# Kernel optimization log

Hardware: AMD Instinct MI355X
Metric: run time of the kernel (lower is better)

The kernel has to match this reference:

```python
import jax, jax.numpy as jnp
import numpy as np

WINDOW_SIZE = 64
SHIFT_SIZE = WINDOW_SIZE // 2  # shift_windows=True
HEAD_DIM = 64
SCALE = HEAD_DIM ** (-0.5)


def _shift_mask(W):
    # static shift-window mask, computed with numpy (all shapes static)
    img_mask = np.zeros((W,), dtype=np.float32)
    cnt = 0
    for s in (slice(0, -WINDOW_SIZE), slice(-WINDOW_SIZE, -SHIFT_SIZE), slice(-SHIFT_SIZE, None)):
        img_mask[s] = cnt
        cnt += 1
    mw = img_mask.reshape(W // WINDOW_SIZE, WINDOW_SIZE)  # (num_win, ws)
    mask = mw[:, None, :] - mw[:, :, None]                # (num_win, ws, ws)
    mask = np.where(mask != 0.0, -100.0, 0.0).astype(np.float32)
    return jnp.asarray(mask)


def setup_inputs() -> dict:
    key = jax.random.key(0)
    k1, k2, k3, k4 = jax.random.split(key, 4)
    B, W, C = 32, 8192, HEAD_DIM
    return {
        "q": jax.random.normal(k1, (B, W, C), dtype=jnp.float32),
        "k": jax.random.normal(k2, (B, W, C), dtype=jnp.float32),
        "v": jax.random.normal(k3, (B, W, C), dtype=jnp.float32),
        "rel_pos_table": jax.random.normal(k4, (2 * WINDOW_SIZE - 1, 1), dtype=jnp.float32) * 0.02,
    }


def reference(q, k, v, rel_pos_table):
    B, W, C = q.shape
    ws = WINDOW_SIZE
    # relative position bias gather: (1, ws, ws)
    coords = jnp.arange(ws)
    rel_idx = coords[None, :] * 0 + (coords[:, None] - coords[None, :]) + (ws - 1)  # (ws, ws)
    bias = rel_pos_table[rel_idx.reshape(-1)].reshape(ws, ws, -1)
    bias = jnp.transpose(bias, (2, 0, 1))  # (1, ws, ws)

    mask = _shift_mask(W)  # (num_win, ws, ws)

    # cyclic shift
    q = jnp.roll(q, shift=-SHIFT_SIZE, axis=1)
    k = jnp.roll(k, shift=-SHIFT_SIZE, axis=1)
    v = jnp.roll(v, shift=-SHIFT_SIZE, axis=1)

    # window partition -> (B * num_win, ws, C)
    num_win = W // ws
    qw = q.reshape(B * num_win, ws, C)
    kw = k.reshape(B * num_win, ws, C)
    vw = v.reshape(B * num_win, ws, C)

    attn = jnp.einsum('bnc,bmc->bnm', qw, kw) * SCALE + bias  # (B*nw, ws, ws)
    attn = attn.reshape(B, num_win, ws, ws) + mask[None]
    attn = attn.reshape(-1, ws, ws)
    attn = jax.nn.softmax(attn, axis=-1)

    xw = jnp.einsum('bnm,bmc->bnc', attn, vw)  # (B*nw, ws, C)
    x = xw.reshape(B, W, C)
    x = jnp.roll(x, shift=SHIFT_SIZE, axis=1)
    return (x, attn)
```

## Files before the change

kernel.cpp:

```cpp
#include <hip/hip_runtime.h>
#include <cstdint>
#include <cstddef>

#define WS 64
#define SHIFT 32
#define WTOT 8192
#define NWIN 128
#define NWPB 8
#define NBLK 512
#define SCALE_F 0.125f

typedef __bf16 bf16x8 __attribute__((ext_vector_type(8)));
typedef __bf16 bf16x4 __attribute__((ext_vector_type(4)));
typedef float f32x4 __attribute__((ext_vector_type(4)));

__device__ __forceinline__ int swz16(int row, int col) {
  return (row * WS + col) ^ (((row >> 1) & 7) << 3);
}

__global__ __launch_bounds__(256, 2) void win_attn(
    const float* __restrict__ q, const float* __restrict__ k,
    const float* __restrict__ v, const float* __restrict__ table,
    float* __restrict__ xout, float* __restrict__ attn_out) {
  __shared__ __align__(16) unsigned short s_mem[2][4 * WS * WS];

  const int t = threadIdx.x;
  const int bid = blockIdx.x;
  const int lane = t & 63;
  const int wave = t >> 6;
  const int lrow = lane & 15;
  const int quad = lane >> 4;

  const int klr = t >> 2;
  const int klc = (t & 3) << 4;
  const int vm0 = (t >> 4) << 2;
  const int vc0 = (t & 15) << 2;

  float biasr[4][4];
  {
    const float* tb = table + (WS - 1);
#pragma unroll
    for (int reg = 0; reg < 4; ++reg) {
      const int r = wave * 16 + quad * 4 + reg;
#pragma unroll
      for (int j = 0; j < 4; ++j) {
        biasr[reg][j] = __ldg(tb + (r - (j * 16 + lrow)));
      }
    }
  }

  float4 L[2][12];

#define ISSUE(W)                                                          \
  {                                                                       \
    const int wid_ = bid * NWPB + (W);                                    \
    const int ba_ = wid_ >> 7;                                            \
    const int wi_ = wid_ & (NWIN - 1);                                    \
    const size_t base_ = (size_t)ba_ * WTOT;                              \
    const int qr_ = (wi_ * WS + wave * 16 + lrow + SHIFT) & (WTOT - 1);   \
    const float* qp_ = q + (base_ + qr_) * WS + quad * 8;                 \
    L[(W) & 1][0] = *(const float4*)(qp_);                                \
    L[(W) & 1][1] = *(const float4*)(qp_ + 4);                            \
    L[(W) & 1][2] = *(const float4*)(qp_ + 32);                           \
    L[(W) & 1][3] = *(const float4*)(qp_ + 36);                           \
    const int kr_ = (wi_ * WS + klr + SHIFT) & (WTOT - 1);                \
    const float* kp_ = k + (base_ + kr_) * WS + klc;                      \
    L[(W) & 1][4] = *(const float4*)(kp_);                                \
    L[(W) & 1][5] = *(const float4*)(kp_ + 4);                            \
    L[(W) & 1][6] = *(const float4*)(kp_ + 8);                            \
    L[(W) & 1][7] = *(const float4*)(kp_ + 12);                           \
    const int vr0_ = (wi_ * WS + vm0 + 0 + SHIFT) & (WTOT - 1);           \
    const int vr1_ = (wi_ * WS + vm0 + 1 + SHIFT) & (WTOT - 1);           \
    const int vr2_ = (wi_ * WS + vm0 + 2 + SHIFT) & (WTOT - 1);           \
    const int vr3_ = (wi_ * WS + vm0 + 3 + SHIFT) & (WTOT - 1);           \
    L[(W) & 1][8]  = *(const float4*)(v + (base_ + vr0_) * WS + vc0);     \
    L[(W) & 1][9]  = *(const float4*)(v + (base_ + vr1_) * WS + vc0);     \
    L[(W) & 1][10] = *(const float4*)(v + (base_ + vr2_) * WS + vc0);     \
    L[(W) & 1][11] = *(const float4*)(v + (base_ + vr3_) * WS + vc0);     \
  }

  ISSUE(0);

#pragma unroll
  for (int w = 0; w < NWPB; ++w) {
    const int s = w & 1;
    unsigned short* const s_khi  = s_mem[s];
    unsigned short* const s_klo  = s_mem[s] + WS * WS;
    unsigned short* const s_vthi = s_mem[s] + 2 * WS * WS;
    unsigned short* const s_vtlo = s_mem[s] + 3 * WS * WS;

    const int wid = bid * NWPB + w;
    const int batch = wid >> 7;
    const int win = wid & (NWIN - 1);
    const bool masked = (win == NWIN - 1);
    const size_t base = (size_t)batch * WTOT;

    if (w + 1 < NWPB) ISSUE(w + 1);

    {
      const float a[16] = {L[s][4].x, L[s][4].y, L[s][4].z, L[s][4].w,
                           L[s][5].x, L[s][5].y, L[s][5].z, L[s][5].w,
                           L[s][6].x, L[s][6].y, L[s][6].z, L[s][6].w,
                           L[s][7].x, L[s][7].y, L[s][7].z, L[s][7].w};
#pragma unroll
      for (int h = 0; h < 2; ++h) {
        bf16x8 hv, lv;
#pragma unroll
        for (int e = 0; e < 8; ++e) {
          const float x = a[8 * h + e];
          const __bf16 hh = (__bf16)x;
          hv[e] = hh;
          lv[e] = (__bf16)(x - (float)hh);
        }
        const int idx = swz16(klr, klc + 8 * h);
        *(bf16x8*)(s_khi + idx) = hv;
        *(bf16x8*)(s_klo + idx) = lv;
      }
    }
    {
      const float vb[4][4] = {
          {L[s][8].x,  L[s][8].y,  L[s][8].z,  L[s][8].w},
          {L[s][9].x,  L[s][9].y,  L[s][9].z,  L[s][9].w},
          {L[s][10].x, L[s][10].y, L[s][10].z, L[s][10].w},
          {L[s][11].x, L[s][11].y, L[s][11].z, L[s][11].w}};
#pragma unroll
      for (int e = 0; e < 4; ++e) {
        bf16x4 hv, lv;
#pragma unroll
        for (int j = 0; j < 4; ++j) {
          const float x = vb[j][e];
          const __bf16 hh = (__bf16)x;
          hv[j] = hh;
          lv[j] = (__bf16)(x - (float)hh);
        }
        const int idx = swz16(vc0 + e, vm0);
        *(bf16x4*)(s_vthi + idx) = hv;
        *(bf16x4*)(s_vtlo + idx) = lv;
      }
    }
    bf16x8 qfhi[2], qflo[2];
#pragma unroll
    for (int kh = 0; kh < 2; ++kh) {
      const float a[8] = {L[s][2 * kh].x,     L[s][2 * kh].y,
                          L[s][2 * kh].z,     L[s][2 * kh].w,
                          L[s][2 * kh + 1].x, L[s][2 * kh + 1].y,
                          L[s][2 * kh + 1].z, L[s][2 * kh + 1].w};
      bf16x8 hv, lv;
#pragma unroll
      for (int e = 0; e < 8; ++e) {
        const __bf16 hh = (__bf16)a[e];
        hv[e] = hh;
        lv[e] = (__bf16)(a[e] - (float)hh);
      }
      qfhi[kh] = hv;
      qflo[kh] = lv;
    }

    __syncthreads();

    const f32x4 z4 = {0.f, 0.f, 0.f, 0.f};
    f32x4 acc[4] = {z4, z4, z4, z4};
#pragma unroll
    for (int kh = 0; kh < 2; ++kh) {
      const int k0 = kh * 32 + quad * 8;
      const bf16x8 ahi = qfhi[kh];
      const bf16x8 alo = qflo[kh];
#pragma unroll
      for (int j = 0; j < 4; ++j) {
        const int idx = swz16(j * 16 + lrow, k0);
        const bf16x8 bhi = *(const bf16x8*)(s_khi + idx);
        const bf16x8 blo = *(const bf16x8*)(s_klo + idx);
        acc[j] = __builtin_amdgcn_mfma_f32_16x16x32_bf16(ahi, bhi, acc[j], 0, 0, 0);
        acc[j] = __builtin_amdgcn_mfma_f32_16x16x32_bf16(alo, bhi, acc[j], 0, 0, 0);
        acc[j] = __builtin_amdgcn_mfma_f32_16x16x32_bf16(ahi, blo, acc[j], 0, 0, 0);
      }
    }

    float p[4][4];
#pragma unroll
    for (int reg = 0; reg < 4; ++reg) {
      const int r = wave * 16 + quad * 4 + reg;
      float val[4];
      float vmax = -1e30f;
#pragma unroll
      for (int j = 0; j < 4; ++j) {
        const int m = j * 16 + lrow;
        float sv = acc[j][reg] * SCALE_F + biasr[reg][j];
        if (masked && (((r ^ m) & 32) != 0)) sv -= 100.0f;
        val[j] = sv;
        vmax = fmaxf(vmax, sv);
      }
#pragma unroll
      for (int off = 1; off < 16; off <<= 1)
        vmax = fmaxf(vmax, __shfl_xor(vmax, off, 64));
      float sum = 0.f;
#pragma unroll
      for (int j = 0; j < 4; ++j) {
        val[j] = __expf(val[j] - vmax);
        sum += val[j];
      }
#pragma unroll
      for (int off = 1; off < 16; off <<= 1)
        sum += __shfl_xor(sum, off, 64);
      const float inv = 1.0f / sum;
#pragma unroll
      for (int j = 0; j < 4; ++j) p[reg][j] = val[j] * inv;
    }

    __syncthreads();

    {
      float* arow = attn_out + (size_t)wid * (WS * WS);
#pragma unroll
      for (int reg = 0; reg < 4; ++reg) {
        const int r = wave * 16 + quad * 4 + reg;
#pragma unroll
        for (int j = 0; j < 4; ++j) {
          const int m = j * 16 + lrow;
          const float pv = p[reg][j];
          arow[r * WS + m] = pv;
          const __bf16 hh = (__bf16)pv;
          const int idx = swz16(r, m);
          *(__bf16*)(s_khi + idx) = hh;
          *(__bf16*)(s_klo + idx) = (__bf16)(pv - (float)hh);
        }
      }
    }
    __syncthreads();

    f32x4 xacc[4] = {z4, z4, z4, z4};
#pragma unroll
    for (int kh = 0; kh < 2; ++kh) {
      const int k0 = kh * 32 + quad * 8;
      const int aidx = swz16(wave * 16 + lrow, k0);
      const bf16x8 phi = *(const bf16x8*)(s_khi + aidx);
      const bf16x8 plo = *(const bf16x8*)(s_klo + aidx);
#pragma unroll
      for (int j = 0; j < 4; ++j) {
        const int idx = swz16(j * 16 + lrow, k0);
        const bf16x8 vhi = *(const bf16x8*)(s_vthi + idx);
        const bf16x8 vlo = *(const bf16x8*)(s_vtlo + idx);
        xacc[j] = __builtin_amdgcn_mfma_f32_16x16x32_bf16(phi, vhi, xacc[j], 0, 0, 0);
        xacc[j] = __builtin_amdgcn_mfma_f32_16x16x32_bf16(plo, vhi, xacc[j], 0, 0, 0);
        xacc[j] = __builtin_amdgcn_mfma_f32_16x16x32_bf16(phi, vlo, xacc[j], 0, 0, 0);
      }
    }

#pragma unroll
    for (int reg = 0; reg < 4; ++reg) {
      const int r = wave * 16 + quad * 4 + reg;
      const int gr = (win * WS + r + SHIFT) & (WTOT - 1);
      float* xrow = xout + (base + gr) * WS;
#pragma unroll
      for (int j = 0; j < 4; ++j) {
        xrow[j * 16 + lrow] = xacc[j][reg];
      }
    }
  }
#undef ISSUE
}

extern "C" void kernel_launch(void* const* d_in, const int* in_sizes, int n_in,
                              void* d_out, int out_size, void* d_ws, size_t ws_size,
                              hipStream_t stream) {
  (void)in_sizes; (void)n_in; (void)out_size; (void)d_ws; (void)ws_size;
  const float* q = (const float*)d_in[0];
  const float* k = (const float*)d_in[1];
  const float* v = (const float*)d_in[2];
  const float* table = (const float*)d_in[3];
  float* xout = (float*)d_out;
  float* attn = (float*)d_out + (size_t)32 * WTOT * WS;
  win_attn<<<dim3(NBLK), dim3(256), 0, stream>>>(q, k, v, table, xout, attn);
}
```

Measured before the change: 290.9 us.

## Stage attn and output tiles through LDS for float4 global stores

Probabilities and output accumulators are now written to a swizzled fp32 LDS tile, then stored to global memory as row-contiguous float4 vectors instead of scattered scalar stores. The P hi/lo bf16 split moves to the PV operand load, LDS drops from double buffering to a single buffer, blocks handle 4 windows each with launch bounds raised to 4 blocks per CU, and barriers wait only on lgkmcnt. This targets store coalescing and occupancy. In exchange it adds LDS round trips and reuses one buffer across windows, which depends on the row-local ordering being correct.

```diff
diff --git a/kernel.cpp b/kernel.cpp
--- a/kernel.cpp
+++ b/kernel.cpp
@@ -6,23 +6,39 @@
 #define SHIFT 32
 #define WTOT 8192
 #define NWIN 128
-#define NWPB 8
-#define NBLK 512
+#define NWPB 4
+#define NBLK 1024
 #define SCALE_F 0.125f
 
 typedef __bf16 bf16x8 __attribute__((ext_vector_type(8)));
 typedef __bf16 bf16x4 __attribute__((ext_vector_type(4)));
 typedef float f32x4 __attribute__((ext_vector_type(4)));
 
+#define BAR_LGKM()                                        \
+  do {                                                    \
+    asm volatile("s_waitcnt lgkmcnt(0)" ::: "memory");    \
+    __builtin_amdgcn_s_barrier();                         \
+    asm volatile("" ::: "memory");                        \
+  } while (0)
+
 __device__ __forceinline__ int swz16(int row, int col) {
   return (row * WS + col) ^ (((row >> 1) & 7) << 3);
 }
-
-__global__ __launch_bounds__(256, 2) void win_attn(
+__device__ __forceinline__ int swz32(int row, int col) {
+  const int q2 = (row >> 2) & 3;
+  return row * WS + (col ^ (((q2 & 1) << 4) | ((q2 >> 1) << 2)));
+}
+
+__global__ __launch_bounds__(256, 4) void win_attn(
     const float* __restrict__ q, const float* __restrict__ k,
     const float* __restrict__ v, const float* __restrict__ table,
     float* __restrict__ xout, float* __restrict__ attn_out) {
-  __shared__ __align__(16) unsigned short s_mem[2][4 * WS * WS];
+  __shared__ __align__(16) unsigned short s_mem[4 * WS * WS];
+  unsigned short* const s_khi  = s_mem;
+  unsigned short* const s_klo  = s_mem + WS * WS;
+  unsigned short* const s_vthi = s_mem + 2 * WS * WS;
+  unsigned short* const s_vtlo = s_mem + 3 * WS * WS;
+  float* const s_p = (float*)s_mem;
 
   const int t = threadIdx.x;
   const int bid = blockIdx.x;
@@ -71,7 +87,7 @@
     L[(W) & 1][7] = *(const float4*)(kp_ + 12);                           \
     const int vr0_ = (wi_ * WS + vm0 + 0 + SHIFT) & (WTOT - 1);           \
     const int vr1_ = (wi_ * WS + vm0 + 1 + SHIFT) & (WTOT - 1);           \
-    const int vr2_ = (wi_ * WS + vm0 + 2 + SHIFT) & (WTOT - 1);           \
+    const int vr2_ = (wi_ * WS + vm0 + 2 + SHIFT) & (WTOT - 1);          \
     const int vr3_ = (wi_ * WS + vm0 + 3 + SHIFT) & (WTOT - 1);           \
     L[(W) & 1][8]  = *(const float4*)(v + (base_ + vr0_) * WS + vc0);     \
     L[(W) & 1][9]  = *(const float4*)(v + (base_ + vr1_) * WS + vc0);     \
@@ -84,11 +100,6 @@
 #pragma unroll
   for (int w = 0; w < NWPB; ++w) {
     const int s = w & 1;
-    unsigned short* const s_khi  = s_mem[s];
-    unsigned short* const s_klo  = s_mem[s] + WS * WS;
-    unsigned short* const s_vthi = s_mem[s] + 2 * WS * WS;
-    unsigned short* const s_vtlo = s_mem[s] + 3 * WS * WS;
-
     const int wid = bid * NWPB + w;
     const int batch = wid >> 7;
     const int win = wid & (NWIN - 1);
@@ -156,7 +167,7 @@
       qflo[kh] = lv;
     }
 
-    __syncthreads();
+    BAR_LGKM();
 
     const f32x4 z4 = {0.f, 0.f, 0.f, 0.f};
     f32x4 acc[4] = {z4, z4, z4, z4};
@@ -207,37 +218,45 @@
       for (int j = 0; j < 4; ++j) p[reg][j] = val[j] * inv;
     }
 
-    __syncthreads();
+    BAR_LGKM();
+
+#pragma unroll
+    for (int reg = 0; reg < 4; ++reg) {
+      const int r = wave * 16 + quad * 4 + reg;
+#pragma unroll
+      for (int j = 0; j < 4; ++j) {
+        s_p[swz32(r, j * 16 + lrow)] = p[reg][j];
+      }
+    }
 
     {
-      float* arow = attn_out + (size_t)wid * (WS * WS);
-#pragma unroll
-      for (int reg = 0; reg < 4; ++reg) {
-        const int r = wave * 16 + quad * 4 + reg;
-#pragma unroll
-        for (int j = 0; j < 4; ++j) {
-          const int m = j * 16 + lrow;
-          const float pv = p[reg][j];
-          arow[r * WS + m] = pv;
-          const __bf16 hh = (__bf16)pv;
-          const int idx = swz16(r, m);
-          *(__bf16*)(s_khi + idx) = hh;
-          *(__bf16*)(s_klo + idx) = (__bf16)(pv - (float)hh);
-        }
-      }
-    }
-    __syncthreads();
+      const int r = wave * 16 + lrow;
+      float* arow = attn_out + (size_t)wid * (WS * WS) + (size_t)r * WS;
+#pragma unroll
+      for (int i = 0; i < 4; ++i) {
+        const int c = i * 16 + quad * 4;
+        *(float4*)(arow + c) = *(const float4*)(s_p + swz32(r, c));
+      }
+    }
 
     f32x4 xacc[4] = {z4, z4, z4, z4};
 #pragma unroll
     for (int kh = 0; kh < 2; ++kh) {
-      const int k0 = kh * 32 + quad * 8;
-      const int aidx = swz16(wave * 16 + lrow, k0);
-      const bf16x8 phi = *(const bf16x8*)(s_khi + aidx);
-      const bf16x8 plo = *(const bf16x8*)(s_klo + aidx);
-#pragma unroll
-      for (int j = 0; j < 4; ++j) {
-        const int idx = swz16(j * 16 + lrow, k0);
+      const int c0 = kh * 32 + quad * 8;
+      const int r = wave * 16 + lrow;
+      const float4 a0 = *(const float4*)(s_p + swz32(r, c0));
+      const float4 a1 = *(const float4*)(s_p + swz32(r, c0 + 4));
+      const float pa[8] = {a0.x, a0.y, a0.z, a0.w, a1.x, a1.y, a1.z, a1.w};
+      bf16x8 phi, plo;
+#pragma unroll
+      for (int e = 0; e < 8; ++e) {
+        const __bf16 h = (__bf16)pa[e];
+        phi[e] = h;
+        plo[e] = (__bf16)(pa[e] - (float)h);
+      }
+#pragma unroll
+      for (int j = 0; j < 4; ++j) {
+        const int idx = swz16(j * 16 + lrow, c0);
         const bf16x8 vhi = *(const bf16x8*)(s_vthi + idx);
         const bf16x8 vlo = *(const bf16x8*)(s_vtlo + idx);
         xacc[j] = __builtin_amdgcn_mfma_f32_16x16x32_bf16(phi, vhi, xacc[j], 0, 0, 0);
@@ -249,13 +268,23 @@
 #pragma unroll
     for (int reg = 0; reg < 4; ++reg) {
       const int r = wave * 16 + quad * 4 + reg;
+#pragma unroll
+      for (int j = 0; j < 4; ++j) {
+        s_p[swz32(r, j * 16 + lrow)] = xacc[j][reg];
+      }
+    }
+    {
+      const int r = wave * 16 + lrow;
       const int gr = (win * WS + r + SHIFT) & (WTOT - 1);
       float* xrow = xout + (base + gr) * WS;
 #pragma unroll
-      for (int j = 0; j < 4; ++j) {
-        xrow[j * 16 + lrow] = xacc[j][reg];
-      }
-    }
+      for (int i = 0; i < 4; ++i) {
+        const int c = i * 16 + quad * 4;
+        *(float4*)(xrow + c) = *(const float4*)(s_p + swz32(r, c));
+      }
+    }
+
+    BAR_LGKM();
   }
 #undef ISSUE
 }
```

New measurement: 303.5 us. 1.04x slower.
